# Kernel optimization log

Measured on AMD Instinct MI355X. Metric: run time of the kernel, lower is better.

The kernel has to match this reference:

```python
import jax, jax.numpy as jnp
import numpy as np

B, N, F, K = 4096, 2048, 64, 64


def setup_inputs() -> dict:
    key = jax.random.key(0)
    k1, k2, k3, k4, k5 = jax.random.split(key, 5)
    X = jax.random.normal(k1, (B, N), dtype=jnp.float32)
    W = jax.random.normal(k2, (1, N), dtype=jnp.float32) * (1.0 / np.sqrt(N))
    b = jax.random.normal(k3, (1,), dtype=jnp.float32)
    vector = jax.random.normal(k4, (N, F, K), dtype=jnp.float32)
    feature2field = jax.random.randint(k5, (N,), 0, F, dtype=jnp.int32)
    return {"X": X, "W": W, "b": b, "vector": vector, "feature2field": feature2field}


def reference(X, W, b, vector, feature2field):
    # linear part: [B, 1]
    linear = X @ W.T + b
    # field-aware latent vector of feature i w.r.t. its own field: V[i] = vector[i, f2f[i]]  -> [N, K]
    V = vector[jnp.arange(vector.shape[0]), feature2field]
    # pairwise latent dot products S[i,j] = <V[i], V[j]>  -> [N, N]
    S = V @ V.T
    # Gram matrix over batch: P[i,j] = sum_b X[b,i] * X[b,j]  -> [N, N]
    P = X.T @ X
    # original loop accumulates sum over i<j and over batch of S[i,j] * X[:,i]*X[:,j],
    # then adds that scalar to every row of the linear output
    triu = jnp.triu(jnp.ones_like(S), k=1)
    interaction = jnp.sum(S * P * triu)
    return linear + interaction
```

## Files before the change

### kernel.cpp

```cpp
#include <hip/hip_runtime.h>

#define NB 4096
#define NN 2048
#define NF 64
#define NK 64

#define NCH 8
#define CLEN 256
#define RPB 64
#define KSTEPS (CLEN / 32)

typedef short bf16x8 __attribute__((ext_vector_type(8)));
typedef float f32x4  __attribute__((ext_vector_type(4)));

#define OFF_VGTH 0
#define OFF_VGTL (OFF_VGTH + NK * NN * 2)
#define OFF_VN   (OFF_VGTL + NK * NN * 2)
#define OFF_LINP (OFF_VN + NN * 4)
#define OFF_DDP  (OFF_LINP + NCH * NB * 4)
#define OFF_SROW (OFF_DDP + NCH * NB * 4)
#define OFF_LINT (OFF_SROW + NB * 4)
#define OFF_TP   (OFF_LINT + NB * 4)

__device__ inline unsigned short bf16_rtn(float f) {
    unsigned u = __float_as_uint(f);
    return (unsigned short)((u + 0x7fffu + ((u >> 16) & 1u)) >> 16);
}

__global__ __launch_bounds__(256) void k_prep(const float* __restrict__ vec,
                                              const int* __restrict__ f2f,
                                              unsigned short* __restrict__ VgTh,
                                              unsigned short* __restrict__ VgTl,
                                              float* __restrict__ vnorm) {
    __shared__ unsigned short tH[64][72];
    __shared__ unsigned short tL[64][72];
    const int t  = threadIdx.x;
    const int i0 = blockIdx.x * 64;
    {
        const int il = t >> 2;
        const int sg = (t & 3) * 16;
        const int i  = i0 + il;
        const int f  = f2f[i];
        const float* p = vec + (size_t)i * (NF * NK) + (size_t)f * NK + sg;
        float nsum = 0.f;
        #pragma unroll
        for (int j4 = 0; j4 < 4; ++j4) {
            float4 v = *reinterpret_cast<const float4*>(p + j4 * 4);
            float vv[4] = {v.x, v.y, v.z, v.w};
            #pragma unroll
            for (int e = 0; e < 4; ++e) {
                float x = vv[e];
                nsum = fmaf(x, x, nsum);
                unsigned xb = __float_as_uint(x);
                float hf = __uint_as_float(xb & 0xffff0000u);
                int k = sg + j4 * 4 + e;
                tH[il][k] = (unsigned short)(xb >> 16);
                tL[il][k] = bf16_rtn(x - hf);
            }
        }
        nsum += __shfl_xor(nsum, 1, 64);
        nsum += __shfl_xor(nsum, 2, 64);
        if ((t & 3) == 0) vnorm[i] = nsum;
    }
    __syncthreads();
    {
        const int k  = t >> 2;
        const int is = (t & 3) * 16;
        unsigned short hb[16], lb[16];
        #pragma unroll
        for (int j = 0; j < 16; ++j) { hb[j] = tH[is + j][k]; lb[j] = tL[is + j][k]; }
        unsigned short* ph = VgTh + (size_t)k * NN + i0 + is;
        unsigned short* pl = VgTl + (size_t)k * NN + i0 + is;
        *reinterpret_cast<uint4*>(ph)     = *reinterpret_cast<uint4*>(hb);
        *reinterpret_cast<uint4*>(ph + 8) = *reinterpret_cast<uint4*>(hb + 8);
        *reinterpret_cast<uint4*>(pl)     = *reinterpret_cast<uint4*>(lb);
        *reinterpret_cast<uint4*>(pl + 8) = *reinterpret_cast<uint4*>(lb + 8);
    }
}

__global__ __launch_bounds__(256, 2) void k_main(const float* __restrict__ X,
                                                 const float* __restrict__ Wg,
                                                 const unsigned short* __restrict__ VgTh,
                                                 const unsigned short* __restrict__ VgTl,
                                                 const float* __restrict__ vn,
                                                 float* __restrict__ Tp,
                                                 float* __restrict__ linp,
                                                 float* __restrict__ ddp) {
    const int t    = threadIdx.x;
    const int lane = t & 63;
    const int w    = t >> 6;
    const int rg   = blockIdx.x >> 3;
    const int ch   = blockIdx.x & 7;
    const int r0   = rg * RPB;
    const int c0   = ch * CLEN;

    const int m    = lane & 15;
    const int quad = lane >> 4;
    const int row  = r0 + w * 16 + m;

    const float* xp = X  + (size_t)row * NN + c0 + quad * 8;
    const float* wp = Wg + c0 + quad * 8;
    const float* np = vn + c0 + quad * 8;

    f32x4 acc[4];
    #pragma unroll
    for (int nt = 0; nt < 4; ++nt)
        #pragma unroll
        for (int e = 0; e < 4; ++e) acc[nt][e] = 0.f;
    float lin = 0.f, dd = 0.f;

    #pragma unroll
    for (int s = 0; s < KSTEPS; ++s) {
        float4 xa = *reinterpret_cast<const float4*>(xp + s * 32);
        float4 xb = *reinterpret_cast<const float4*>(xp + s * 32 + 4);
        float4 wa = *reinterpret_cast<const float4*>(wp + s * 32);
        float4 wb = *reinterpret_cast<const float4*>(wp + s * 32 + 4);
        float4 na = *reinterpret_cast<const float4*>(np + s * 32);
        float4 nb = *reinterpret_cast<const float4*>(np + s * 32 + 4);

        float xs8[8] = {xa.x, xa.y, xa.z, xa.w, xb.x, xb.y, xb.z, xb.w};
        float ws8[8] = {wa.x, wa.y, wa.z, wa.w, wb.x, wb.y, wb.z, wb.w};
        float ns8[8] = {na.x, na.y, na.z, na.w, nb.x, nb.y, nb.z, nb.w};

        #pragma unroll
        for (int j = 0; j < 8; ++j) {
            lin = fmaf(xs8[j], ws8[j], lin);
            dd  = fmaf(xs8[j] * xs8[j], ns8[j], dd);
        }

        bf16x8 ah, al;
        #pragma unroll
        for (int j = 0; j < 8; ++j) {
            unsigned ub = __float_as_uint(xs8[j]);
            ah[j] = (short)(ub >> 16);
            float hf = __uint_as_float(ub & 0xffff0000u);
            al[j] = (short)bf16_rtn(xs8[j] - hf);
        }

        const size_t boff = (size_t)c0 + s * 32 + quad * 8;
        #pragma unroll
        for (int nt = 0; nt < 4; ++nt) {
            const size_t nrow = (size_t)(nt * 16 + m) * NN + boff;
            bf16x8 bh = *reinterpret_cast<const bf16x8*>(VgTh + nrow);
            bf16x8 bl = *reinterpret_cast<const bf16x8*>(VgTl + nrow);
            acc[nt] = __builtin_amdgcn_mfma_f32_16x16x32_bf16(ah, bh, acc[nt], 0, 0, 0);
            acc[nt] = __builtin_amdgcn_mfma_f32_16x16x32_bf16(al, bh, acc[nt], 0, 0, 0);
            acc[nt] = __builtin_amdgcn_mfma_f32_16x16x32_bf16(ah, bl, acc[nt], 0, 0, 0);
        }
    }

    lin += __shfl_xor(lin, 16, 64);
    lin += __shfl_xor(lin, 32, 64);
    dd  += __shfl_xor(dd, 16, 64);
    dd  += __shfl_xor(dd, 32, 64);
    if (quad == 0) {
        linp[ch * NB + row] = lin;
        ddp [ch * NB + row] = dd;
    }

    float* tb = Tp + (size_t)ch * NB * NK;
    #pragma unroll
    for (int nt = 0; nt < 4; ++nt)
        #pragma unroll
        for (int r = 0; r < 4; ++r) {
            int rr = r0 + w * 16 + quad * 4 + r;
            tb[(size_t)rr * NK + nt * 16 + m] = acc[nt][r];
        }
}

__global__ __launch_bounds__(256) void k_red(const float* __restrict__ Tp,
                                             const float* __restrict__ linp,
                                             const float* __restrict__ ddp,
                                             float* __restrict__ srow,
                                             float* __restrict__ lint) {
    int gid = blockIdx.x * 256 + threadIdx.x;
    int row = gid >> 4;
    int g   = gid & 15;
    float4 s = {0.f, 0.f, 0.f, 0.f};
    #pragma unroll
    for (int cc = 0; cc < NCH; ++cc) {
        float4 p = *reinterpret_cast<const float4*>(
            Tp + ((size_t)cc * NB + row) * NK + g * 4);
        s.x += p.x; s.y += p.y; s.z += p.z; s.w += p.w;
    }
    float v = s.x * s.x + s.y * s.y + s.z * s.z + s.w * s.w;
    float l = (g < NCH) ? linp[g * NB + row] : 0.f;
    float d = (g < NCH) ? ddp [g * NB + row] : 0.f;
    #pragma unroll
    for (int mm = 1; mm < 16; mm <<= 1) {
        v += __shfl_xor(v, mm, 64);
        l += __shfl_xor(l, mm, 64);
        d += __shfl_xor(d, mm, 64);
    }
    if (g == 0) { srow[row] = v - d; lint[row] = l; }
}

__global__ __launch_bounds__(256) void k_final(const float* __restrict__ lint,
                                               const float* __restrict__ srow,
                                               const float* __restrict__ bptr,
                                               float* __restrict__ out) {
    __shared__ double red[256];
    int t = threadIdx.x;
    double a = 0.0;
    for (int j = t; j < NB; j += 256) a += (double)srow[j];
    red[t] = a;
    __syncthreads();
    #pragma unroll
    for (int s = 128; s; s >>= 1) {
        if (t < s) red[t] += red[t + s];
        __syncthreads();
    }
    float inter = (float)(0.5 * red[0]);
    float bias  = bptr[0];
    for (int j = t; j < NB; j += 256) out[j] = lint[j] + bias + inter;
}

extern "C" void kernel_launch(void* const* d_in, const int* in_sizes, int n_in,
                              void* d_out, int out_size, void* d_ws, size_t ws_size,
                              hipStream_t stream) {
    const float* X    = (const float*)d_in[0];
    const float* W    = (const float*)d_in[1];
    const float* bias = (const float*)d_in[2];
    const float* vec  = (const float*)d_in[3];
    const int*   f2f  = (const int*)d_in[4];
    float* out = (float*)d_out;

    char* base = (char*)d_ws;
    unsigned short* VgTh = (unsigned short*)(base + OFF_VGTH);
    unsigned short* VgTl = (unsigned short*)(base + OFF_VGTL);
    float* vnorm = (float*)(base + OFF_VN);
    float* linp  = (float*)(base + OFF_LINP);
    float* ddp   = (float*)(base + OFF_DDP);
    float* srow  = (float*)(base + OFF_SROW);
    float* lint  = (float*)(base + OFF_LINT);
    float* Tp    = (float*)(base + OFF_TP);

    k_prep<<<NN / 64, 256, 0, stream>>>(vec, f2f, VgTh, VgTl, vnorm);
    k_main<<<(NB / RPB) * NCH, 256, 0, stream>>>(X, W, VgTh, VgTl, vnorm,
                                                 Tp, linp, ddp);
    k_red<<<NB * 16 / 256, 256, 0, stream>>>(Tp, linp, ddp, srow, lint);
    k_final<<<1, 256, 0, stream>>>(lint, srow, bias, out);
}
```

Baseline: 127.8 us.

## Fuse chunk reduction and final sum into main kernel via LDS and last-block atomic

Each block now handles 16 rows across the full feature dimension with 16 waves splitting the columns. Per-wave MFMA partials are reduced in shared memory instead of being written to a global Tp buffer and reduced by a separate kernel. The global scalar sum is done by the last block, chosen through an atomic counter that k_prep resets. This removes two kernel launches and the round trip of partials through global memory. In exchange it relies on threadfence/atomic ordering, runs 256 blocks of 1024 threads with heavy LDS use (which limits occupancy), and reads the V tiles once per row block.

```diff
diff --git a/kernel.cpp b/kernel.cpp
--- a/kernel.cpp
+++ b/kernel.cpp
@@ -5,10 +5,12 @@
 #define NF 64
 #define NK 64
 
-#define NCH 8
-#define CLEN 256
-#define RPB 64
-#define KSTEPS (CLEN / 32)
+#define RPB   16
+#define TPB   1024
+#define NWAVE 16
+#define CPW   (NN / NWAVE)
+#define KS    (CPW / 32)
+#define GRID  (NB / RPB)
 
 typedef short bf16x8 __attribute__((ext_vector_type(8)));
 typedef float f32x4  __attribute__((ext_vector_type(4)));
@@ -16,11 +18,9 @@
 #define OFF_VGTH 0
 #define OFF_VGTL (OFF_VGTH + NK * NN * 2)
 #define OFF_VN   (OFF_VGTL + NK * NN * 2)
-#define OFF_LINP (OFF_VN + NN * 4)
-#define OFF_DDP  (OFF_LINP + NCH * NB * 4)
-#define OFF_SROW (OFF_DDP + NCH * NB * 4)
-#define OFF_LINT (OFF_SROW + NB * 4)
-#define OFF_TP   (OFF_LINT + NB * 4)
+#define OFF_LINT (OFF_VN + NN * 4)
+#define OFF_BP   (OFF_LINT + NB * 4)
+#define OFF_CNT  (OFF_BP + GRID * 8)
 
 __device__ inline unsigned short bf16_rtn(float f) {
     unsigned u = __float_as_uint(f);
@@ -31,11 +31,13 @@
                                               const int* __restrict__ f2f,
                                               unsigned short* __restrict__ VgTh,
                                               unsigned short* __restrict__ VgTl,
-                                              float* __restrict__ vnorm) {
+                                              float* __restrict__ vnorm,
+                                              unsigned* __restrict__ cnt) {
     __shared__ unsigned short tH[64][72];
     __shared__ unsigned short tL[64][72];
     const int t  = threadIdx.x;
     const int i0 = blockIdx.x * 64;
+    if (blockIdx.x == 0 && t == 0) *cnt = 0u;
     {
         const int il = t >> 2;
         const int sg = (t & 3) * 16;
@@ -78,29 +80,37 @@
     }
 }
 
-__global__ __launch_bounds__(256, 2) void k_main(const float* __restrict__ X,
-                                                 const float* __restrict__ Wg,
-                                                 const unsigned short* __restrict__ VgTh,
-                                                 const unsigned short* __restrict__ VgTl,
-                                                 const float* __restrict__ vn,
-                                                 float* __restrict__ Tp,
-                                                 float* __restrict__ linp,
-                                                 float* __restrict__ ddp) {
+__global__ __launch_bounds__(TPB) void k_main(const float* __restrict__ X,
+                                              const float* __restrict__ Wg,
+                                              const unsigned short* __restrict__ VgTh,
+                                              const unsigned short* __restrict__ VgTl,
+                                              const float* __restrict__ vn,
+                                              const float* __restrict__ bptr,
+                                              float* __restrict__ lint,
+                                              double* __restrict__ bpart,
+                                              unsigned* __restrict__ cnt,
+                                              float* __restrict__ out) {
+    __shared__ float Tl[NWAVE * 1088];
+    __shared__ float linW[NWAVE * 17];
+    __shared__ float ddW[NWAVE * 17];
+    __shared__ float rowRes[RPB];
+    __shared__ float interS;
+    __shared__ int   lastS;
+
     const int t    = threadIdx.x;
+    const int w    = t >> 6;
     const int lane = t & 63;
-    const int w    = t >> 6;
-    const int rg   = blockIdx.x >> 3;
-    const int ch   = blockIdx.x & 7;
-    const int r0   = rg * RPB;
-    const int c0   = ch * CLEN;
-
     const int m    = lane & 15;
     const int quad = lane >> 4;
-    const int row  = r0 + w * 16 + m;
-
-    const float* xp = X  + (size_t)row * NN + c0 + quad * 8;
-    const float* wp = Wg + c0 + quad * 8;
-    const float* np = vn + c0 + quad * 8;
+    const int r0   = blockIdx.x * RPB;
+    const int row  = r0 + m;
+    const int cw   = w * CPW;
+
+    const float* xp = X  + (size_t)row * NN + cw + quad * 8;
+    const float* wp = Wg + cw + quad * 8;
+    const float* np = vn + cw + quad * 8;
+    const unsigned short* bhp = VgTh + (size_t)m * NN + cw + quad * 8;
+    const unsigned short* blp = VgTl + (size_t)m * NN + cw + quad * 8;
 
     f32x4 acc[4];
     #pragma unroll
@@ -110,7 +120,7 @@
     float lin = 0.f, dd = 0.f;
 
     #pragma unroll
-    for (int s = 0; s < KSTEPS; ++s) {
+    for (int s = 0; s < KS; ++s) {
         float4 xa = *reinterpret_cast<const float4*>(xp + s * 32);
         float4 xb = *reinterpret_cast<const float4*>(xp + s * 32 + 4);
         float4 wa = *reinterpret_cast<const float4*>(wp + s * 32);
@@ -137,82 +147,80 @@
             al[j] = (short)bf16_rtn(xs8[j] - hf);
         }
 
-        const size_t boff = (size_t)c0 + s * 32 + quad * 8;
         #pragma unroll
         for (int nt = 0; nt < 4; ++nt) {
-            const size_t nrow = (size_t)(nt * 16 + m) * NN + boff;
-            bf16x8 bh = *reinterpret_cast<const bf16x8*>(VgTh + nrow);
-            bf16x8 bl = *reinterpret_cast<const bf16x8*>(VgTl + nrow);
+            bf16x8 bh = *reinterpret_cast<const bf16x8*>(bhp + (size_t)nt * 16 * NN + s * 32);
+            bf16x8 bl = *reinterpret_cast<const bf16x8*>(blp + (size_t)nt * 16 * NN + s * 32);
             acc[nt] = __builtin_amdgcn_mfma_f32_16x16x32_bf16(ah, bh, acc[nt], 0, 0, 0);
             acc[nt] = __builtin_amdgcn_mfma_f32_16x16x32_bf16(al, bh, acc[nt], 0, 0, 0);
             acc[nt] = __builtin_amdgcn_mfma_f32_16x16x32_bf16(ah, bl, acc[nt], 0, 0, 0);
         }
     }
 
-    lin += __shfl_xor(lin, 16, 64);
-    lin += __shfl_xor(lin, 32, 64);
-    dd  += __shfl_xor(dd, 16, 64);
-    dd  += __shfl_xor(dd, 32, 64);
-    if (quad == 0) {
-        linp[ch * NB + row] = lin;
-        ddp [ch * NB + row] = dd;
-    }
-
-    float* tb = Tp + (size_t)ch * NB * NK;
     #pragma unroll
     for (int nt = 0; nt < 4; ++nt)
         #pragma unroll
-        for (int r = 0; r < 4; ++r) {
-            int rr = r0 + w * 16 + quad * 4 + r;
-            tb[(size_t)rr * NK + nt * 16 + m] = acc[nt][r];
-        }
-}
-
-__global__ __launch_bounds__(256) void k_red(const float* __restrict__ Tp,
-                                             const float* __restrict__ linp,
-                                             const float* __restrict__ ddp,
-                                             float* __restrict__ srow,
-                                             float* __restrict__ lint) {
-    int gid = blockIdx.x * 256 + threadIdx.x;
-    int row = gid >> 4;
-    int g   = gid & 15;
-    float4 s = {0.f, 0.f, 0.f, 0.f};
-    #pragma unroll
-    for (int cc = 0; cc < NCH; ++cc) {
-        float4 p = *reinterpret_cast<const float4*>(
-            Tp + ((size_t)cc * NB + row) * NK + g * 4);
-        s.x += p.x; s.y += p.y; s.z += p.z; s.w += p.w;
-    }
-    float v = s.x * s.x + s.y * s.y + s.z * s.z + s.w * s.w;
-    float l = (g < NCH) ? linp[g * NB + row] : 0.f;
-    float d = (g < NCH) ? ddp [g * NB + row] : 0.f;
-    #pragma unroll
-    for (int mm = 1; mm < 16; mm <<= 1) {
-        v += __shfl_xor(v, mm, 64);
-        l += __shfl_xor(l, mm, 64);
-        d += __shfl_xor(d, mm, 64);
-    }
-    if (g == 0) { srow[row] = v - d; lint[row] = l; }
-}
-
-__global__ __launch_bounds__(256) void k_final(const float* __restrict__ lint,
-                                               const float* __restrict__ srow,
-                                               const float* __restrict__ bptr,
-                                               float* __restrict__ out) {
-    __shared__ double red[256];
-    int t = threadIdx.x;
-    double a = 0.0;
-    for (int j = t; j < NB; j += 256) a += (double)srow[j];
-    red[t] = a;
-    __syncthreads();
-    #pragma unroll
-    for (int s = 128; s; s >>= 1) {
-        if (t < s) red[t] += red[t + s];
+        for (int r = 0; r < 4; ++r)
+            Tl[w * 1088 + (quad * 4 + r) * 68 + nt * 16 + m] = acc[nt][r];
+
+    lin += __shfl_xor(lin, 16, 64); lin += __shfl_xor(lin, 32, 64);
+    dd  += __shfl_xor(dd, 16, 64);  dd  += __shfl_xor(dd, 32, 64);
+    if (quad == 0) { linW[w * 17 + m] = lin; ddW[w * 17 + m] = dd; }
+    __syncthreads();
+
+    {
+        float ts = 0.f;
+        #pragma unroll
+        for (int ww = 0; ww < NWAVE; ++ww)
+            ts += Tl[ww * 1088 + w * 68 + lane];
+        float s2 = ts * ts;
+        #pragma unroll
+        for (int d = 1; d < 64; d <<= 1) s2 += __shfl_xor(s2, d, 64);
+        float lw = (lane < 16) ? linW[lane * 17 + w] : 0.f;
+        float dw = (lane < 16) ? ddW [lane * 17 + w] : 0.f;
+        #pragma unroll
+        for (int d = 1; d < 16; d <<= 1) {
+            lw += __shfl_xor(lw, d, 64);
+            dw += __shfl_xor(dw, d, 64);
+        }
+        if (lane == 0) {
+            lint[r0 + w] = lw;
+            rowRes[w]    = s2 - dw;
+        }
+    }
+    __syncthreads();
+
+    if (t == 0) {
+        double p = 0.0;
+        #pragma unroll
+        for (int r = 0; r < RPB; ++r) p += (double)rowRes[r];
+        bpart[blockIdx.x] = p;
+    }
+    __threadfence();
+    __syncthreads();
+    if (t == 0) {
+        unsigned old = atomicAdd(cnt, 1u);
+        lastS = (old == GRID - 1) ? 1 : 0;
+    }
+    __syncthreads();
+
+    if (lastS) {
+        __threadfence();
+        if (w == 0) {
+            double p = 0.0;
+            #pragma unroll
+            for (int j = 0; j < 4; ++j) p += bpart[lane * 4 + j];
+            #pragma unroll
+            for (int d = 1; d < 64; d <<= 1) p += __shfl_xor(p, d, 64);
+            if (lane == 0) interS = (float)(0.5 * p);
+        }
         __syncthreads();
-    }
-    float inter = (float)(0.5 * red[0]);
-    float bias  = bptr[0];
-    for (int j = t; j < NB; j += 256) out[j] = lint[j] + bias + inter;
+        float inter = interS;
+        float bias  = bptr[0];
+        #pragma unroll
+        for (int j = 0; j < NB / TPB; ++j)
+            out[t + j * TPB] = lint[t + j * TPB] + bias + inter;
+    }
 }
 
 extern "C" void kernel_launch(void* const* d_in, const int* in_sizes, int n_in,
@@ -228,16 +236,12 @@
     char* base = (char*)d_ws;
     unsigned short* VgTh = (unsigned short*)(base + OFF_VGTH);
     unsigned short* VgTl = (unsigned short*)(base + OFF_VGTL);
-    float* vnorm = (float*)(base + OFF_VN);
-    float* linp  = (float*)(base + OFF_LINP);
-    float* ddp   = (float*)(base + OFF_DDP);
-    float* srow  = (float*)(base + OFF_SROW);
-    float* lint  = (float*)(base + OFF_LINT);
-    float* Tp    = (float*)(base + OFF_TP);
-
-    k_prep<<<NN / 64, 256, 0, stream>>>(vec, f2f, VgTh, VgTl, vnorm);
-    k_main<<<(NB / RPB) * NCH, 256, 0, stream>>>(X, W, VgTh, VgTl, vnorm,
-                                                 Tp, linp, ddp);
-    k_red<<<NB * 16 / 256, 256, 0, stream>>>(Tp, linp, ddp, srow, lint);
-    k_final<<<1, 256, 0, stream>>>(lint, srow, bias, out);
-}
+    float*    vnorm = (float*)   (base + OFF_VN);
+    float*    lint  = (float*)   (base + OFF_LINT);
+    double*   bpart = (double*)  (base + OFF_BP);
+    unsigned* cnt   = (unsigned*)(base + OFF_CNT);
+
+    k_prep<<<NN / 64, 256, 0, stream>>>(vec, f2f, VgTh, VgTl, vnorm, cnt);
+    k_main<<<GRID, TPB, 0, stream>>>(X, W, VgTh, VgTl, vnorm, bias,
+                                     lint, bpart, cnt, out);
+}
```

Measured after the change: 180.7 us. 1.41x slower.

## Split K into 16 chunks, prefetch operands, fold final reduction via atomics

Applied to the files above, without the earlier changes.

Doubles the number of column chunks (CLEN 256→128) so the main kernel launches twice as many blocks, and raises the occupancy hint to 4 blocks per CU. Operands for the next k-step (X row data and the bf16 hi/lo V tiles) are now loaded one iteration ahead in software. The single-block double-precision final reduction is replaced by per-block partial sums in the reduction kernel, combined with a float atomicAdd into a scalar zeroed in the prep kernel, and a wide elementwise final kernel. The trade-offs are a larger partial-result buffer to write and re-read, possible register pressure under the tighter launch bound, and a nondeterministic float32 accumulation order for the interaction scalar.

```diff
diff --git a/kernel.cpp b/kernel.cpp
--- a/kernel.cpp
+++ b/kernel.cpp
@@ -5,10 +5,11 @@
 #define NF 64
 #define NK 64
 
-#define NCH 8
-#define CLEN 256
+#define NCH 16
+#define CLEN 128
+#define KS (CLEN / 32)
 #define RPB 64
-#define KSTEPS (CLEN / 32)
+#define GRID ((NB / RPB) * NCH)
 
 typedef short bf16x8 __attribute__((ext_vector_type(8)));
 typedef float f32x4  __attribute__((ext_vector_type(4)));
@@ -16,11 +17,11 @@
 #define OFF_VGTH 0
 #define OFF_VGTL (OFF_VGTH + NK * NN * 2)
 #define OFF_VN   (OFF_VGTL + NK * NN * 2)
-#define OFF_LINP (OFF_VN + NN * 4)
+#define OFF_LINT (OFF_VN + NN * 4)
+#define OFF_LINP (OFF_LINT + NB * 4)
 #define OFF_DDP  (OFF_LINP + NCH * NB * 4)
-#define OFF_SROW (OFF_DDP + NCH * NB * 4)
-#define OFF_LINT (OFF_SROW + NB * 4)
-#define OFF_TP   (OFF_LINT + NB * 4)
+#define OFF_STOT (OFF_DDP + NCH * NB * 4)
+#define OFF_TP   (OFF_STOT + 256)
 
 __device__ inline unsigned short bf16_rtn(float f) {
     unsigned u = __float_as_uint(f);
@@ -31,11 +32,13 @@
                                               const int* __restrict__ f2f,
                                               unsigned short* __restrict__ VgTh,
                                               unsigned short* __restrict__ VgTl,
-                                              float* __restrict__ vnorm) {
+                                              float* __restrict__ vnorm,
+                                              float* __restrict__ stot) {
     __shared__ unsigned short tH[64][72];
     __shared__ unsigned short tL[64][72];
     const int t  = threadIdx.x;
     const int i0 = blockIdx.x * 64;
+    if (blockIdx.x == 0 && t == 0) *stot = 0.f;
     {
         const int il = t >> 2;
         const int sg = (t & 3) * 16;
@@ -78,7 +81,7 @@
     }
 }
 
-__global__ __launch_bounds__(256, 2) void k_main(const float* __restrict__ X,
+__global__ __launch_bounds__(256, 4) void k_main(const float* __restrict__ X,
                                                  const float* __restrict__ Wg,
                                                  const unsigned short* __restrict__ VgTh,
                                                  const unsigned short* __restrict__ VgTl,
@@ -89,8 +92,8 @@
     const int t    = threadIdx.x;
     const int lane = t & 63;
     const int w    = t >> 6;
-    const int rg   = blockIdx.x >> 3;
-    const int ch   = blockIdx.x & 7;
+    const int rg   = blockIdx.x >> 4;
+    const int ch   = blockIdx.x & 15;
     const int r0   = rg * RPB;
     const int c0   = ch * CLEN;
 
@@ -101,6 +104,8 @@
     const float* xp = X  + (size_t)row * NN + c0 + quad * 8;
     const float* wp = Wg + c0 + quad * 8;
     const float* np = vn + c0 + quad * 8;
+    const unsigned short* bhp = VgTh + (size_t)m * NN + c0 + quad * 8;
+    const unsigned short* blp = VgTl + (size_t)m * NN + c0 + quad * 8;
 
     f32x4 acc[4];
     #pragma unroll
@@ -109,10 +114,27 @@
         for (int e = 0; e < 4; ++e) acc[nt][e] = 0.f;
     float lin = 0.f, dd = 0.f;
 
-    #pragma unroll
-    for (int s = 0; s < KSTEPS; ++s) {
-        float4 xa = *reinterpret_cast<const float4*>(xp + s * 32);
-        float4 xb = *reinterpret_cast<const float4*>(xp + s * 32 + 4);
+    float4 xa = *reinterpret_cast<const float4*>(xp);
+    float4 xb = *reinterpret_cast<const float4*>(xp + 4);
+    bf16x8 cbh[4], cbl[4];
+    #pragma unroll
+    for (int nt = 0; nt < 4; ++nt) {
+        cbh[nt] = *reinterpret_cast<const bf16x8*>(bhp + (size_t)nt * 16 * NN);
+        cbl[nt] = *reinterpret_cast<const bf16x8*>(blp + (size_t)nt * 16 * NN);
+    }
+
+    #pragma unroll
+    for (int s = 0; s < KS; ++s) {
+        const int sn = (s + 1 < KS) ? s + 1 : s;
+        float4 xaN = *reinterpret_cast<const float4*>(xp + sn * 32);
+        float4 xbN = *reinterpret_cast<const float4*>(xp + sn * 32 + 4);
+        bf16x8 nbh[4], nbl[4];
+        #pragma unroll
+        for (int nt = 0; nt < 4; ++nt) {
+            nbh[nt] = *reinterpret_cast<const bf16x8*>(bhp + (size_t)nt * 16 * NN + sn * 32);
+            nbl[nt] = *reinterpret_cast<const bf16x8*>(blp + (size_t)nt * 16 * NN + sn * 32);
+        }
+
         float4 wa = *reinterpret_cast<const float4*>(wp + s * 32);
         float4 wb = *reinterpret_cast<const float4*>(wp + s * 32 + 4);
         float4 na = *reinterpret_cast<const float4*>(np + s * 32);
@@ -137,22 +159,20 @@
             al[j] = (short)bf16_rtn(xs8[j] - hf);
         }
 
-        const size_t boff = (size_t)c0 + s * 32 + quad * 8;
         #pragma unroll
         for (int nt = 0; nt < 4; ++nt) {
-            const size_t nrow = (size_t)(nt * 16 + m) * NN + boff;
-            bf16x8 bh = *reinterpret_cast<const bf16x8*>(VgTh + nrow);
-            bf16x8 bl = *reinterpret_cast<const bf16x8*>(VgTl + nrow);
-            acc[nt] = __builtin_amdgcn_mfma_f32_16x16x32_bf16(ah, bh, acc[nt], 0, 0, 0);
-            acc[nt] = __builtin_amdgcn_mfma_f32_16x16x32_bf16(al, bh, acc[nt], 0, 0, 0);
-            acc[nt] = __builtin_amdgcn_mfma_f32_16x16x32_bf16(ah, bl, acc[nt], 0, 0, 0);
-        }
-    }
-
-    lin += __shfl_xor(lin, 16, 64);
-    lin += __shfl_xor(lin, 32, 64);
-    dd  += __shfl_xor(dd, 16, 64);
-    dd  += __shfl_xor(dd, 32, 64);
+            acc[nt] = __builtin_amdgcn_mfma_f32_16x16x32_bf16(ah, cbh[nt], acc[nt], 0, 0, 0);
+            acc[nt] = __builtin_amdgcn_mfma_f32_16x16x32_bf16(al, cbh[nt], acc[nt], 0, 0, 0);
+            acc[nt] = __builtin_amdgcn_mfma_f32_16x16x32_bf16(ah, cbl[nt], acc[nt], 0, 0, 0);
+        }
+
+        xa = xaN; xb = xbN;
+        #pragma unroll
+        for (int nt = 0; nt < 4; ++nt) { cbh[nt] = nbh[nt]; cbl[nt] = nbl[nt]; }
+    }
+
+    lin += __shfl_xor(lin, 16, 64); lin += __shfl_xor(lin, 32, 64);
+    dd  += __shfl_xor(dd, 16, 64);  dd  += __shfl_xor(dd, 32, 64);
     if (quad == 0) {
         linp[ch * NB + row] = lin;
         ddp [ch * NB + row] = dd;
@@ -171,8 +191,9 @@
 __global__ __launch_bounds__(256) void k_red(const float* __restrict__ Tp,
                                              const float* __restrict__ linp,
                                              const float* __restrict__ ddp,
-                                             float* __restrict__ srow,
-                                             float* __restrict__ lint) {
+                                             float* __restrict__ lint,
+                                             float* __restrict__ stot) {
+    __shared__ float bp[4];
     int gid = blockIdx.x * 256 + threadIdx.x;
     int row = gid >> 4;
     int g   = gid & 15;
@@ -184,35 +205,30 @@
         s.x += p.x; s.y += p.y; s.z += p.z; s.w += p.w;
     }
     float v = s.x * s.x + s.y * s.y + s.z * s.z + s.w * s.w;
-    float l = (g < NCH) ? linp[g * NB + row] : 0.f;
-    float d = (g < NCH) ? ddp [g * NB + row] : 0.f;
+    float l = linp[g * NB + row];
+    float d = ddp [g * NB + row];
     #pragma unroll
     for (int mm = 1; mm < 16; mm <<= 1) {
         v += __shfl_xor(v, mm, 64);
         l += __shfl_xor(l, mm, 64);
         d += __shfl_xor(d, mm, 64);
     }
-    if (g == 0) { srow[row] = v - d; lint[row] = l; }
+    float sr = (g == 0) ? (v - d) : 0.f;
+    if (g == 0) lint[row] = l;
+    sr += __shfl_xor(sr, 16, 64);
+    sr += __shfl_xor(sr, 32, 64);
+    if ((threadIdx.x & 63) == 0) bp[threadIdx.x >> 6] = sr;
+    __syncthreads();
+    if (threadIdx.x == 0)
+        atomicAdd(stot, bp[0] + bp[1] + bp[2] + bp[3]);
 }
 
 __global__ __launch_bounds__(256) void k_final(const float* __restrict__ lint,
-                                               const float* __restrict__ srow,
+                                               const float* __restrict__ stot,
                                                const float* __restrict__ bptr,
                                                float* __restrict__ out) {
-    __shared__ double red[256];
-    int t = threadIdx.x;
-    double a = 0.0;
-    for (int j = t; j < NB; j += 256) a += (double)srow[j];
-    red[t] = a;
-    __syncthreads();
-    #pragma unroll
-    for (int s = 128; s; s >>= 1) {
-        if (t < s) red[t] += red[t + s];
-        __syncthreads();
-    }
-    float inter = (float)(0.5 * red[0]);
-    float bias  = bptr[0];
-    for (int j = t; j < NB; j += 256) out[j] = lint[j] + bias + inter;
+    int b = blockIdx.x * 256 + threadIdx.x;
+    out[b] = lint[b] + bptr[0] + 0.5f * stot[0];
 }
 
 extern "C" void kernel_launch(void* const* d_in, const int* in_sizes, int n_in,
@@ -229,15 +245,14 @@
     unsigned short* VgTh = (unsigned short*)(base + OFF_VGTH);
     unsigned short* VgTl = (unsigned short*)(base + OFF_VGTL);
     float* vnorm = (float*)(base + OFF_VN);
+    float* lint  = (float*)(base + OFF_LINT);
     float* linp  = (float*)(base + OFF_LINP);
     float* ddp   = (float*)(base + OFF_DDP);
-    float* srow  = (float*)(base + OFF_SROW);
-    float* lint  = (float*)(base + OFF_LINT);
+    float* stot  = (float*)(base + OFF_STOT);
     float* Tp    = (float*)(base + OFF_TP);
 
-    k_prep<<<NN / 64, 256, 0, stream>>>(vec, f2f, VgTh, VgTl, vnorm);
-    k_main<<<(NB / RPB) * NCH, 256, 0, stream>>>(X, W, VgTh, VgTl, vnorm,
-                                                 Tp, linp, ddp);
-    k_red<<<NB * 16 / 256, 256, 0, stream>>>(Tp, linp, ddp, srow, lint);
-    k_final<<<1, 256, 0, stream>>>(lint, srow, bias, out);
-}
+    k_prep<<<NN / 64, 256, 0, stream>>>(vec, f2f, VgTh, VgTl, vnorm, stot);
+    k_main<<<GRID, 256, 0, stream>>>(X, W, VgTh, VgTl, vnorm, Tp, linp, ddp);
+    k_red<<<NB * 16 / 256, 256, 0, stream>>>(Tp, linp, ddp, lint, stot);
+    k_final<<<NB / 256, 256, 0, stream>>>(lint, stot, bias, out);
+}
```

After: 125.4 us. No clear change (-1.9%).
